# Kernel tuning notes

Measured on AMD Instinct MI355X. Metric: run time of the kernel, lower is better.

Reference implementation:

```python
import jax, jax.numpy as jnp
import numpy as np

EPS = 1e-12
NUM_ITERATIONS = 3


def squash(t, axis=-1):
    sn = jnp.sum(t * t, axis=axis, keepdims=True)
    scale = sn / (1.0 + sn + EPS)
    return scale * t / jnp.sqrt(sn + EPS)


def setup_inputs() -> dict:
    key = jax.random.key(0)
    k1, k2 = jax.random.split(key)
    B, R, IN, OUT, C = 128, 4096, 16, 32, 2
    x = jax.random.normal(k1, (B, R, IN), dtype=jnp.float32)
    # learned parameter: torch.randn(num_capsules, num_route_nodes, in, out)
    route_weights = jax.random.normal(k2, (C, R, IN, OUT), dtype=jnp.float32)
    return {"x": x, "route_weights": route_weights}


def reference(x, route_weights):
    # priors: [C, B, R, 1, O] == x[None,:,:,None,:] @ W[:,None,:,:,:]
    priors = jnp.einsum('bri,crio->cbro', x, route_weights)[..., None, :]
    # logits kept [C,B,R,1,1]: the torch code stores [C,B,R,1,O] but every
    # update (delta_logits) is constant along O, so softmax over axis=2 is identical.
    logits = jnp.zeros(priors.shape[:-1] + (1,), dtype=priors.dtype)
    outputs = None
    for i in range(NUM_ITERATIONS):
        probs = jax.nn.softmax(logits, axis=2)                      # over route nodes
        s = jnp.sum(probs * priors, axis=2, keepdims=True)          # [C,B,1,1,O]
        outputs = squash(s, axis=-1)
        if i != NUM_ITERATIONS - 1:
            delta = jnp.sum(priors * outputs, axis=-1, keepdims=True)  # [C,B,R,1,1]
            logits = logits + delta
    return outputs
```

## Files before the change

### kernel.cpp

```cpp
#include <hip/hip_runtime.h>
#include <hip/hip_cooperative_groups.h>
#include <math.h>

namespace cg = cooperative_groups;

#define CB    128
#define CR    4096
#define CIN   16
#define COUT  32
#define CCAP  2
#define RC    16
#define NRCH  (CR / RC)
#define GRID  (CCAP * NRCH)
#define EPSF  1e-12f

typedef _Float16 h8  __attribute__((ext_vector_type(8)));
typedef _Float16 h4t __attribute__((ext_vector_type(4)));
typedef float    f4  __attribute__((ext_vector_type(4)));
typedef float    f8v __attribute__((ext_vector_type(8)));

__device__ __forceinline__ void stage_pack_W(const float* __restrict__ w,
                                             int c, int r0, int t,
                                             _Float16* WpL, float* Stg)
{
  h4t* WpL4 = (h4t*)WpL;
#pragma unroll
  for (int h = 0; h < 2; ++h) {
    const float4* src = (const float4*)(w + ((size_t)c * CR + r0 + h * 8) * 512);
    ((float4*)Stg)[t]       = src[t];
    ((float4*)Stg)[t + 512] = src[t + 512];
    __syncthreads();
#pragma unroll
    for (int q = 0; q < 2; ++q) {
      const int sl  = t * 2 + q;
      const int rr  = sl >> 7;
      const int rem = sl & 127;
      const int ot  = rem >> 6;
      const int gs  = (rem >> 4) & 3;
      const int ms  = rem & 15;
      h4t v;
#pragma unroll
      for (int j = 0; j < 4; ++j)
        v[j] = (_Float16)Stg[rr * 512 + (4 * gs + j) * 32 + ot * 16 + ms];
      WpL4[(h * 8 + rr) * 128 + rem] = v;
    }
    __syncthreads();
  }
}

__device__ __forceinline__ void store_partials(float* __restrict__ partialA,
                                               float* __restrict__ partialE,
                                               const float* accA, const float* accB,
                                               float esum, int c, int rch,
                                               int t, int g, int b)
{
  float4 a4 = {accA[0], accA[1], accA[2], accA[3]};
  float4 b4 = {accB[0], accB[1], accB[2], accB[3]};
  float* dst = partialA + ((size_t)(c * NRCH + rch)) * 4096 + (size_t)t * 8;
  *(float4*)dst = a4;
  *(float4*)(dst + 4) = b4;
  if (g == 0) partialE[((size_t)(c * NRCH + rch)) * CB + b] = esum;
}

__device__ __forceinline__ void pass0_body(const float* __restrict__ x,
                                           float* __restrict__ partialA,
                                           float* __restrict__ partialE,
                                           const _Float16* WpL,
                                           int c, int rch, int t, h8* pf)
{
  const int r0 = rch * RC;
  const int wv = t >> 6, L = t & 63, g = L >> 4, m = L & 15;
  const int b  = wv * 16 + m;
  const h4t* WpL4 = (const h4t*)WpL;

  float accA[4] = {0.f, 0.f, 0.f, 0.f};
  float accB[4] = {0.f, 0.f, 0.f, 0.f};

#pragma unroll 4
  for (int ri = 0; ri < RC; ++ri) {
    const int r = r0 + ri;
    float4 xf = *(const float4*)(x + ((size_t)b * CR + r) * CIN + 4 * g);
    h8 bx = {(_Float16)xf.x, (_Float16)xf.y, (_Float16)xf.z, (_Float16)xf.w,
             (_Float16)0.f, (_Float16)0.f, (_Float16)0.f, (_Float16)0.f};
    h4t wA4 = WpL4[ri * 128 + L];
    h4t wB4 = WpL4[ri * 128 + 64 + L];
    h8 aA = {wA4[0], wA4[1], wA4[2], wA4[3],
             (_Float16)0.f, (_Float16)0.f, (_Float16)0.f, (_Float16)0.f};
    h8 aB = {wB4[0], wB4[1], wB4[2], wB4[3],
             (_Float16)0.f, (_Float16)0.f, (_Float16)0.f, (_Float16)0.f};
    f4 z = {0.f, 0.f, 0.f, 0.f};
    f4 pA = __builtin_amdgcn_mfma_f32_16x16x32_f16(aA, bx, z, 0, 0, 0);
    f4 pB = __builtin_amdgcn_mfma_f32_16x16x32_f16(aB, bx, z, 0, 0, 0);

    h8 pk = {(_Float16)pA[0], (_Float16)pA[1], (_Float16)pA[2], (_Float16)pA[3],
             (_Float16)pB[0], (_Float16)pB[1], (_Float16)pB[2], (_Float16)pB[3]};
    pf[ri] = pk;
#pragma unroll
    for (int j = 0; j < 4; ++j) { accA[j] += pA[j]; accB[j] += pB[j]; }
  }
  store_partials(partialA, partialE, accA, accB, (float)RC, c, rch, t, g, b);
}

__device__ __forceinline__ void passN_body(const float* __restrict__ vsum,
                                           float* __restrict__ partialA,
                                           float* __restrict__ partialE,
                                           int c, int rch, int t, const h8* pf)
{
  const int wv = t >> 6, L = t & 63, g = L >> 4, m = L & 15;
  const int b  = wv * 16 + m;

  const float* vb = vsum + ((size_t)c * CB + b) * COUT;
  float4 vA = *(const float4*)(vb + 4 * g);
  float4 vB = *(const float4*)(vb + 16 + 4 * g);

  float accA[4] = {0.f, 0.f, 0.f, 0.f};
  float accB[4] = {0.f, 0.f, 0.f, 0.f};
  float esum = 0.f;

#pragma unroll
  for (int ri = 0; ri < RC; ++ri) {
    f8v p = __builtin_convertvector(pf[ri], f8v);
    float d = p[0] * vA.x + p[1] * vA.y + p[2] * vA.z + p[3] * vA.w
            + p[4] * vB.x + p[5] * vB.y + p[6] * vB.z + p[7] * vB.w;
    d += __shfl_xor(d, 16);
    d += __shfl_xor(d, 32);
    const float e = __expf(d);
    esum += e;
#pragma unroll
    for (int j = 0; j < 4; ++j) { accA[j] += e * p[j]; accB[j] += e * p[4 + j]; }
  }
  store_partials(partialA, partialE, accA, accB, esum, c, rch, t, g, b);
}

template <int JG>
__device__ __forceinline__ void redv_body(const float* __restrict__ partialA,
                                          const float* __restrict__ partialE,
                                          float* __restrict__ vsum,
                                          float* __restrict__ out,
                                          float (*red)[33], float* rede,
                                          int cb, int t, int mode)
{
  const int c2 = cb >> 7, b2 = cb & 127;
  const int o = t & 31, jg = t >> 5;
  const int wv2 = b2 >> 4, m2 = b2 & 15;
  const int half = o >> 4, oo = o & 15, g2 = oo >> 2, j2 = oo & 3;
  const size_t idx = (size_t)(wv2 * 64 + g2 * 16 + m2) * 8 + half * 4 + j2;

  float s = 0.f;
#pragma unroll 4
  for (int k = 0; k < NRCH / JG; ++k) {
    const int j = jg + k * JG;
    s += partialA[((size_t)(c2 * NRCH + j)) * 4096 + idx];
  }
  red[jg][o] = s;
  __syncthreads();

  if (t < JG) {
    float e = 0.f;
#pragma unroll 4
    for (int k = 0; k < NRCH / JG; ++k)
      e += partialE[((size_t)(c2 * NRCH + t + k * JG)) * CB + b2];
    rede[t] = e;
  }
  __syncthreads();

  if (t < 32) {
    float sv = 0.f, es = 0.f;
#pragma unroll
    for (int jj = 0; jj < JG; ++jj) { sv += red[jj][t]; es += rede[jj]; }
    float sm = sv / es;
    float sn = sm * sm;
#pragma unroll
    for (int sh = 1; sh < 32; sh <<= 1) sn += __shfl_xor(sn, sh);
    float fac = sn / ((1.f + sn + EPSF) * sqrtf(sn + EPSF));
    float vv = sm * fac;
    if (mode == 2)      out[cb * COUT + t]  = vv;
    else if (mode == 1) vsum[cb * COUT + t] += vv;
    else                vsum[cb * COUT + t] = vv;
  }
}

__global__ __launch_bounds__(512, 4) void caps_coop_kernel(
    const float* __restrict__ x, const float* __restrict__ w,
    float* __restrict__ vsum, float* __restrict__ partialA,
    float* __restrict__ partialE, float* __restrict__ out)
{
  cg::grid_group grid = cg::this_grid();
  const int blk = (int)blockIdx.x;
  const int c = blk >> 8, rch = blk & 255;
  const int t = (int)threadIdx.x;

  __shared__ __align__(16) char lds[32768];
  _Float16* WpL = (_Float16*)lds;
  float* Stg = (float*)(lds + 16384);
  float (*red)[33] = (float (*)[33])(lds + 16384);
  float* rede = (float*)(lds + 16384 + 16 * 33 * 4);

  h8 pf[RC];

  stage_pack_W(w, c, rch * RC, t, WpL, Stg);
  pass0_body(x, partialA, partialE, WpL, c, rch, t, pf);
  __threadfence();
  grid.sync();
  if (blk < 256)
    redv_body<16>(partialA, partialE, vsum, out, red, rede, blk, t, 0);
  __threadfence();
  grid.sync();

#pragma unroll 1
  for (int it = 1; it < 3; ++it) {
    passN_body(vsum, partialA, partialE, c, rch, t, pf);
    __threadfence();
    grid.sync();
    if (blk < 256)
      redv_body<16>(partialA, partialE, vsum, out, red, rede, blk, t, it);
    if (it < 2) {
      __threadfence();
      grid.sync();
    }
  }
}

__device__ __forceinline__ void pass_full_body(const float* __restrict__ x,
                                               const float* __restrict__ vsum,
                                               float* __restrict__ partialA,
                                               float* __restrict__ partialE,
                                               const _Float16* WpL,
                                               int c, int rch, int t, int uniform)
{
  const int r0 = rch * RC;
  const int wv = t >> 6, L = t & 63, g = L >> 4, m = L & 15;
  const int b  = wv * 16 + m;
  const h4t* WpL4 = (const h4t*)WpL;

  float4 vA = {0.f, 0.f, 0.f, 0.f}, vB = {0.f, 0.f, 0.f, 0.f};
  if (!uniform) {
    const float* vb = vsum + ((size_t)c * CB + b) * COUT;
    vA = *(const float4*)(vb + 4 * g);
    vB = *(const float4*)(vb + 16 + 4 * g);
  }
  float accA[4] = {0.f, 0.f, 0.f, 0.f};
  float accB[4] = {0.f, 0.f, 0.f, 0.f};
  float esum = 0.f;

#pragma unroll 4
  for (int ri = 0; ri < RC; ++ri) {
    const int r = r0 + ri;
    float4 xf = *(const float4*)(x + ((size_t)b * CR + r) * CIN + 4 * g);
    h8 bx = {(_Float16)xf.x, (_Float16)xf.y, (_Float16)xf.z, (_Float16)xf.w,
             (_Float16)0.f, (_Float16)0.f, (_Float16)0.f, (_Float16)0.f};
    h4t wA4 = WpL4[ri * 128 + L];
    h4t wB4 = WpL4[ri * 128 + 64 + L];
    h8 aA = {wA4[0], wA4[1], wA4[2], wA4[3],
             (_Float16)0.f, (_Float16)0.f, (_Float16)0.f, (_Float16)0.f};
    h8 aB = {wB4[0], wB4[1], wB4[2], wB4[3],
             (_Float16)0.f, (_Float16)0.f, (_Float16)0.f, (_Float16)0.f};
    f4 z = {0.f, 0.f, 0.f, 0.f};
    f4 pA = __builtin_amdgcn_mfma_f32_16x16x32_f16(aA, bx, z, 0, 0, 0);
    f4 pB = __builtin_amdgcn_mfma_f32_16x16x32_f16(aB, bx, z, 0, 0, 0);

    float e = 1.f;
    if (!uniform) {
      float d = pA[0] * vA.x + pA[1] * vA.y + pA[2] * vA.z + pA[3] * vA.w
              + pB[0] * vB.x + pB[1] * vB.y + pB[2] * vB.z + pB[3] * vB.w;
      d += __shfl_xor(d, 16);
      d += __shfl_xor(d, 32);
      e = __expf(d);
    }
    esum += e;
#pragma unroll
    for (int j = 0; j < 4; ++j) { accA[j] += e * pA[j]; accB[j] += e * pB[j]; }
  }
  store_partials(partialA, partialE, accA, accB, esum, c, rch, t, g, b);
}

__global__ __launch_bounds__(512) void caps_pass_kernel(
    const float* __restrict__ x, const float* __restrict__ w,
    const float* __restrict__ vsum, float* __restrict__ partialA,
    float* __restrict__ partialE, int uniform)
{
  const int blk = (int)blockIdx.x;
  const int c = blk >> 8, rch = blk & 255;
  const int t = (int)threadIdx.x;
  __shared__ __align__(16) char lds[32768];
  _Float16* WpL = (_Float16*)lds;
  float* Stg = (float*)(lds + 16384);
  stage_pack_W(w, c, rch * RC, t, WpL, Stg);
  pass_full_body(x, vsum, partialA, partialE, WpL, c, rch, t, uniform);
}

__global__ __launch_bounds__(256) void caps_redv_kernel(
    const float* __restrict__ partialA, const float* __restrict__ partialE,
    float* __restrict__ vsum, float* __restrict__ out, int mode)
{
  __shared__ float red[8][33];
  __shared__ float rede[8];
  redv_body<8>(partialA, partialE, vsum, out, red, rede,
               (int)blockIdx.x, (int)threadIdx.x, mode);
}

extern "C" void kernel_launch(void* const* d_in, const int* in_sizes, int n_in,
                              void* d_out, int out_size, void* d_ws, size_t ws_size,
                              hipStream_t stream) {
  const float* x = (const float*)d_in[0];
  const float* w = (const float*)d_in[1];
  float* out = (float*)d_out;

  char* p = (char*)d_ws;
  float* vsum = (float*)p;
  p += (size_t)CCAP * CB * COUT * sizeof(float);
  float* partialA = (float*)p;
  p += (size_t)CCAP * NRCH * 4096 * sizeof(float);
  float* partialE = (float*)p;

  int maxB = 0;
  bool coop_ok =
      (hipOccupancyMaxActiveBlocksPerMultiprocessor(
           &maxB, (const void*)caps_coop_kernel, 512, 0) == hipSuccess) &&
      (maxB >= 2);

  if (coop_ok) {
    void* args[] = {(void*)&x, (void*)&w, (void*)&vsum,
                    (void*)&partialA, (void*)&partialE, (void*)&out};
    hipError_t e = hipLaunchCooperativeKernel((const void*)caps_coop_kernel,
                                              dim3(GRID), dim3(512), args, 0,
                                              stream);
    if (e == hipSuccess) return;
    (void)hipGetLastError();
  }

  for (int it = 0; it < 3; ++it) {
    caps_pass_kernel<<<dim3(GRID), 512, 0, stream>>>(
        x, w, vsum, partialA, partialE, it == 0 ? 1 : 0);
    caps_redv_kernel<<<dim3(CCAP * CB), 256, 0, stream>>>(
        partialA, partialE, vsum, out, it);
  }
}
```

Measured before the change: 75.96 us.

## Process both capsules per block in cooperative kernel, halving grid size

The cooperative kernel now launches one block per route chunk (256 blocks) instead of one per capsule-chunk pair (512). Each block stages both capsules' weights into LDS and reuses each x load for both capsules' MFMAs. It also holds priors for both capsules in registers. Every block now takes part in the reduction step instead of only half of them. This halves x global reads and the number of grid-sync participants, but doubles per-thread register use (launch bounds drop to 2 blocks/SM) and raises LDS usage.

```diff
diff --git a/kernel.cpp b/kernel.cpp
--- a/kernel.cpp
+++ b/kernel.cpp
@@ -11,7 +11,6 @@
 #define CCAP  2
 #define RC    16
 #define NRCH  (CR / RC)
-#define GRID  (CCAP * NRCH)
 #define EPSF  1e-12f
 
 typedef _Float16 h8  __attribute__((ext_vector_type(8)));
@@ -62,19 +61,180 @@
   if (g == 0) partialE[((size_t)(c * NRCH + rch)) * CB + b] = esum;
 }
 
-__device__ __forceinline__ void pass0_body(const float* __restrict__ x,
-                                           float* __restrict__ partialA,
-                                           float* __restrict__ partialE,
-                                           const _Float16* WpL,
-                                           int c, int rch, int t, h8* pf)
+template <int JG>
+__device__ __forceinline__ void redv_body(const float* __restrict__ partialA,
+                                          const float* __restrict__ partialE,
+                                          float* __restrict__ vsum,
+                                          float* __restrict__ out,
+                                          float (*red)[33], float* rede,
+                                          int cb, int t, int mode)
+{
+  const int c2 = cb >> 7, b2 = cb & 127;
+  const int o = t & 31, jg = t >> 5;
+  const int wv2 = b2 >> 4, m2 = b2 & 15;
+  const int half = o >> 4, oo = o & 15, g2 = oo >> 2, j2 = oo & 3;
+  const size_t idx = (size_t)(wv2 * 64 + g2 * 16 + m2) * 8 + half * 4 + j2;
+
+  float s = 0.f;
+#pragma unroll 4
+  for (int k = 0; k < NRCH / JG; ++k) {
+    const int j = jg + k * JG;
+    s += partialA[((size_t)(c2 * NRCH + j)) * 4096 + idx];
+  }
+  red[jg][o] = s;
+  __syncthreads();
+
+  if (t < JG) {
+    float e = 0.f;
+#pragma unroll 4
+    for (int k = 0; k < NRCH / JG; ++k)
+      e += partialE[((size_t)(c2 * NRCH + t + k * JG)) * CB + b2];
+    rede[t] = e;
+  }
+  __syncthreads();
+
+  if (t < 32) {
+    float sv = 0.f, es = 0.f;
+#pragma unroll
+    for (int jj = 0; jj < JG; ++jj) { sv += red[jj][t]; es += rede[jj]; }
+    float sm = sv / es;
+    float sn = sm * sm;
+#pragma unroll
+    for (int sh = 1; sh < 32; sh <<= 1) sn += __shfl_xor(sn, sh);
+    float fac = sn / ((1.f + sn + EPSF) * sqrtf(sn + EPSF));
+    float vv = sm * fac;
+    if (mode == 2)      out[cb * COUT + t]  = vv;
+    else if (mode == 1) vsum[cb * COUT + t] += vv;
+    else                vsum[cb * COUT + t] = vv;
+  }
+  __syncthreads();
+}
+
+__global__ __launch_bounds__(512, 2) void caps_coop_kernel(
+    const float* __restrict__ x, const float* __restrict__ w,
+    float* __restrict__ vsum, float* __restrict__ partialA,
+    float* __restrict__ partialE, float* __restrict__ out)
+{
+  cg::grid_group grid = cg::this_grid();
+  const int rch = (int)blockIdx.x;
+  const int r0  = rch * RC;
+  const int t   = (int)threadIdx.x;
+  const int wv  = t >> 6, L = t & 63, g = L >> 4, m = L & 15;
+  const int b   = wv * 16 + m;
+
+  __shared__ __align__(16) char lds[49152];
+  _Float16* WpL0 = (_Float16*)lds;
+  _Float16* WpL1 = (_Float16*)(lds + 16384);
+  float* Stg = (float*)(lds + 32768);
+  float (*red)[33] = (float (*)[33])(lds + 32768);
+  float* rede = (float*)(lds + 32768 + 16 * 33 * 4);
+
+  stage_pack_W(w, 0, r0, t, WpL0, Stg);
+  stage_pack_W(w, 1, r0, t, WpL1, Stg);
+
+  h8 pf0[RC], pf1[RC];
+
+  {
+    const h4t* W0 = (const h4t*)WpL0;
+    const h4t* W1 = (const h4t*)WpL1;
+    float acc0A[4] = {0.f, 0.f, 0.f, 0.f}, acc0B[4] = {0.f, 0.f, 0.f, 0.f};
+    float acc1A[4] = {0.f, 0.f, 0.f, 0.f}, acc1B[4] = {0.f, 0.f, 0.f, 0.f};
+#pragma unroll
+    for (int ri = 0; ri < RC; ++ri) {
+      float4 xf = *(const float4*)(x + ((size_t)b * CR + r0 + ri) * CIN + 4 * g);
+      h8 bx = {(_Float16)xf.x, (_Float16)xf.y, (_Float16)xf.z, (_Float16)xf.w,
+               (_Float16)0.f, (_Float16)0.f, (_Float16)0.f, (_Float16)0.f};
+      f4 z = {0.f, 0.f, 0.f, 0.f};
+
+      h4t a0 = W0[ri * 128 + L], b0 = W0[ri * 128 + 64 + L];
+      h8 aA0 = {a0[0], a0[1], a0[2], a0[3],
+                (_Float16)0.f, (_Float16)0.f, (_Float16)0.f, (_Float16)0.f};
+      h8 aB0 = {b0[0], b0[1], b0[2], b0[3],
+                (_Float16)0.f, (_Float16)0.f, (_Float16)0.f, (_Float16)0.f};
+      f4 pA0 = __builtin_amdgcn_mfma_f32_16x16x32_f16(aA0, bx, z, 0, 0, 0);
+      f4 pB0 = __builtin_amdgcn_mfma_f32_16x16x32_f16(aB0, bx, z, 0, 0, 0);
+      pf0[ri] = h8{(_Float16)pA0[0], (_Float16)pA0[1], (_Float16)pA0[2], (_Float16)pA0[3],
+                   (_Float16)pB0[0], (_Float16)pB0[1], (_Float16)pB0[2], (_Float16)pB0[3]};
+#pragma unroll
+      for (int j = 0; j < 4; ++j) { acc0A[j] += pA0[j]; acc0B[j] += pB0[j]; }
+
+      h4t a1 = W1[ri * 128 + L], b1 = W1[ri * 128 + 64 + L];
+      h8 aA1 = {a1[0], a1[1], a1[2], a1[3],
+                (_Float16)0.f, (_Float16)0.f, (_Float16)0.f, (_Float16)0.f};
+      h8 aB1 = {b1[0], b1[1], b1[2], b1[3],
+                (_Float16)0.f, (_Float16)0.f, (_Float16)0.f, (_Float16)0.f};
+      f4 pA1 = __builtin_amdgcn_mfma_f32_16x16x32_f16(aA1, bx, z, 0, 0, 0);
+      f4 pB1 = __builtin_amdgcn_mfma_f32_16x16x32_f16(aB1, bx, z, 0, 0, 0);
+      pf1[ri] = h8{(_Float16)pA1[0], (_Float16)pA1[1], (_Float16)pA1[2], (_Float16)pA1[3],
+                   (_Float16)pB1[0], (_Float16)pB1[1], (_Float16)pB1[2], (_Float16)pB1[3]};
+#pragma unroll
+      for (int j = 0; j < 4; ++j) { acc1A[j] += pA1[j]; acc1B[j] += pB1[j]; }
+    }
+    store_partials(partialA, partialE, acc0A, acc0B, (float)RC, 0, rch, t, g, b);
+    store_partials(partialA, partialE, acc1A, acc1B, (float)RC, 1, rch, t, g, b);
+  }
+
+  __threadfence();
+  grid.sync();
+  redv_body<16>(partialA, partialE, vsum, out, red, rede, rch, t, 0);
+  __threadfence();
+  grid.sync();
+
+#pragma unroll 1
+  for (int it = 1; it < 3; ++it) {
+#pragma unroll
+    for (int cc = 0; cc < 2; ++cc) {
+      const float* vb = vsum + ((size_t)cc * CB + b) * COUT;
+      float4 vA = *(const float4*)(vb + 4 * g);
+      float4 vB = *(const float4*)(vb + 16 + 4 * g);
+      float accA[4] = {0.f, 0.f, 0.f, 0.f};
+      float accB[4] = {0.f, 0.f, 0.f, 0.f};
+      float esum = 0.f;
+#pragma unroll
+      for (int ri = 0; ri < RC; ++ri) {
+        f8v p = __builtin_convertvector(cc == 0 ? pf0[ri] : pf1[ri], f8v);
+        float d = p[0] * vA.x + p[1] * vA.y + p[2] * vA.z + p[3] * vA.w
+                + p[4] * vB.x + p[5] * vB.y + p[6] * vB.z + p[7] * vB.w;
+        d += __shfl_xor(d, 16);
+        d += __shfl_xor(d, 32);
+        const float e = __expf(d);
+        esum += e;
+#pragma unroll
+        for (int j = 0; j < 4; ++j) { accA[j] += e * p[j]; accB[j] += e * p[4 + j]; }
+      }
+      store_partials(partialA, partialE, accA, accB, esum, cc, rch, t, g, b);
+    }
+    __threadfence();
+    grid.sync();
+    redv_body<16>(partialA, partialE, vsum, out, red, rede, rch, t, it);
+    if (it < 2) {
+      __threadfence();
+      grid.sync();
+    }
+  }
+}
+
+__device__ __forceinline__ void pass_full_body(const float* __restrict__ x,
+                                               const float* __restrict__ vsum,
+                                               float* __restrict__ partialA,
+                                               float* __restrict__ partialE,
+                                               const _Float16* WpL,
+                                               int c, int rch, int t, int uniform)
 {
   const int r0 = rch * RC;
   const int wv = t >> 6, L = t & 63, g = L >> 4, m = L & 15;
   const int b  = wv * 16 + m;
   const h4t* WpL4 = (const h4t*)WpL;
 
+  float4 vA = {0.f, 0.f, 0.f, 0.f}, vB = {0.f, 0.f, 0.f, 0.f};
+  if (!uniform) {
+    const float* vb = vsum + ((size_t)c * CB + b) * COUT;
+    vA = *(const float4*)(vb + 4 * g);
+    vB = *(const float4*)(vb + 16 + 4 * g);
+  }
   float accA[4] = {0.f, 0.f, 0.f, 0.f};
   float accB[4] = {0.f, 0.f, 0.f, 0.f};
+  float esum = 0.f;
 
 #pragma unroll 4
   for (int ri = 0; ri < RC; ++ri) {
@@ -92,173 +252,6 @@
     f4 pA = __builtin_amdgcn_mfma_f32_16x16x32_f16(aA, bx, z, 0, 0, 0);
     f4 pB = __builtin_amdgcn_mfma_f32_16x16x32_f16(aB, bx, z, 0, 0, 0);
 
-    h8 pk = {(_Float16)pA[0], (_Float16)pA[1], (_Float16)pA[2], (_Float16)pA[3],
-             (_Float16)pB[0], (_Float16)pB[1], (_Float16)pB[2], (_Float16)pB[3]};
-    pf[ri] = pk;
-#pragma unroll
-    for (int j = 0; j < 4; ++j) { accA[j] += pA[j]; accB[j] += pB[j]; }
-  }
-  store_partials(partialA, partialE, accA, accB, (float)RC, c, rch, t, g, b);
-}
-
-__device__ __forceinline__ void passN_body(const float* __restrict__ vsum,
-                                           float* __restrict__ partialA,
-                                           float* __restrict__ partialE,
-                                           int c, int rch, int t, const h8* pf)
-{
-  const int wv = t >> 6, L = t & 63, g = L >> 4, m = L & 15;
-  const int b  = wv * 16 + m;
-
-  const float* vb = vsum + ((size_t)c * CB + b) * COUT;
-  float4 vA = *(const float4*)(vb + 4 * g);
-  float4 vB = *(const float4*)(vb + 16 + 4 * g);
-
-  float accA[4] = {0.f, 0.f, 0.f, 0.f};
-  float accB[4] = {0.f, 0.f, 0.f, 0.f};
-  float esum = 0.f;
-
-#pragma unroll
-  for (int ri = 0; ri < RC; ++ri) {
-    f8v p = __builtin_convertvector(pf[ri], f8v);
-    float d = p[0] * vA.x + p[1] * vA.y + p[2] * vA.z + p[3] * vA.w
-            + p[4] * vB.x + p[5] * vB.y + p[6] * vB.z + p[7] * vB.w;
-    d += __shfl_xor(d, 16);
-    d += __shfl_xor(d, 32);
-    const float e = __expf(d);
-    esum += e;
-#pragma unroll
-    for (int j = 0; j < 4; ++j) { accA[j] += e * p[j]; accB[j] += e * p[4 + j]; }
-  }
-  store_partials(partialA, partialE, accA, accB, esum, c, rch, t, g, b);
-}
-
-template <int JG>
-__device__ __forceinline__ void redv_body(const float* __restrict__ partialA,
-                                          const float* __restrict__ partialE,
-                                          float* __restrict__ vsum,
-                                          float* __restrict__ out,
-                                          float (*red)[33], float* rede,
-                                          int cb, int t, int mode)
-{
-  const int c2 = cb >> 7, b2 = cb & 127;
-  const int o = t & 31, jg = t >> 5;
-  const int wv2 = b2 >> 4, m2 = b2 & 15;
-  const int half = o >> 4, oo = o & 15, g2 = oo >> 2, j2 = oo & 3;
-  const size_t idx = (size_t)(wv2 * 64 + g2 * 16 + m2) * 8 + half * 4 + j2;
-
-  float s = 0.f;
-#pragma unroll 4
-  for (int k = 0; k < NRCH / JG; ++k) {
-    const int j = jg + k * JG;
-    s += partialA[((size_t)(c2 * NRCH + j)) * 4096 + idx];
-  }
-  red[jg][o] = s;
-  __syncthreads();
-
-  if (t < JG) {
-    float e = 0.f;
-#pragma unroll 4
-    for (int k = 0; k < NRCH / JG; ++k)
-      e += partialE[((size_t)(c2 * NRCH + t + k * JG)) * CB + b2];
-    rede[t] = e;
-  }
-  __syncthreads();
-
-  if (t < 32) {
-    float sv = 0.f, es = 0.f;
-#pragma unroll
-    for (int jj = 0; jj < JG; ++jj) { sv += red[jj][t]; es += rede[jj]; }
-    float sm = sv / es;
-    float sn = sm * sm;
-#pragma unroll
-    for (int sh = 1; sh < 32; sh <<= 1) sn += __shfl_xor(sn, sh);
-    float fac = sn / ((1.f + sn + EPSF) * sqrtf(sn + EPSF));
-    float vv = sm * fac;
-    if (mode == 2)      out[cb * COUT + t]  = vv;
-    else if (mode == 1) vsum[cb * COUT + t] += vv;
-    else                vsum[cb * COUT + t] = vv;
-  }
-}
-
-__global__ __launch_bounds__(512, 4) void caps_coop_kernel(
-    const float* __restrict__ x, const float* __restrict__ w,
-    float* __restrict__ vsum, float* __restrict__ partialA,
-    float* __restrict__ partialE, float* __restrict__ out)
-{
-  cg::grid_group grid = cg::this_grid();
-  const int blk = (int)blockIdx.x;
-  const int c = blk >> 8, rch = blk & 255;
-  const int t = (int)threadIdx.x;
-
-  __shared__ __align__(16) char lds[32768];
-  _Float16* WpL = (_Float16*)lds;
-  float* Stg = (float*)(lds + 16384);
-  float (*red)[33] = (float (*)[33])(lds + 16384);
-  float* rede = (float*)(lds + 16384 + 16 * 33 * 4);
-
-  h8 pf[RC];
-
-  stage_pack_W(w, c, rch * RC, t, WpL, Stg);
-  pass0_body(x, partialA, partialE, WpL, c, rch, t, pf);
-  __threadfence();
-  grid.sync();
-  if (blk < 256)
-    redv_body<16>(partialA, partialE, vsum, out, red, rede, blk, t, 0);
-  __threadfence();
-  grid.sync();
-
-#pragma unroll 1
-  for (int it = 1; it < 3; ++it) {
-    passN_body(vsum, partialA, partialE, c, rch, t, pf);
-    __threadfence();
-    grid.sync();
-    if (blk < 256)
-      redv_body<16>(partialA, partialE, vsum, out, red, rede, blk, t, it);
-    if (it < 2) {
-      __threadfence();
-      grid.sync();
-    }
-  }
-}
-
-__device__ __forceinline__ void pass_full_body(const float* __restrict__ x,
-                                               const float* __restrict__ vsum,
-                                               float* __restrict__ partialA,
-                                               float* __restrict__ partialE,
-                                               const _Float16* WpL,
-                                               int c, int rch, int t, int uniform)
-{
-  const int r0 = rch * RC;
-  const int wv = t >> 6, L = t & 63, g = L >> 4, m = L & 15;
-  const int b  = wv * 16 + m;
-  const h4t* WpL4 = (const h4t*)WpL;
-
-  float4 vA = {0.f, 0.f, 0.f, 0.f}, vB = {0.f, 0.f, 0.f, 0.f};
-  if (!uniform) {
-    const float* vb = vsum + ((size_t)c * CB + b) * COUT;
-    vA = *(const float4*)(vb + 4 * g);
-    vB = *(const float4*)(vb + 16 + 4 * g);
-  }
-  float accA[4] = {0.f, 0.f, 0.f, 0.f};
-  float accB[4] = {0.f, 0.f, 0.f, 0.f};
-  float esum = 0.f;
-
-#pragma unroll 4
-  for (int ri = 0; ri < RC; ++ri) {
-    const int r = r0 + ri;
-    float4 xf = *(const float4*)(x + ((size_t)b * CR + r) * CIN + 4 * g);
-    h8 bx = {(_Float16)xf.x, (_Float16)xf.y, (_Float16)xf.z, (_Float16)xf.w,
-             (_Float16)0.f, (_Float16)0.f, (_Float16)0.f, (_Float16)0.f};
-    h4t wA4 = WpL4[ri * 128 + L];
-    h4t wB4 = WpL4[ri * 128 + 64 + L];
-    h8 aA = {wA4[0], wA4[1], wA4[2], wA4[3],
-             (_Float16)0.f, (_Float16)0.f, (_Float16)0.f, (_Float16)0.f};
-    h8 aB = {wB4[0], wB4[1], wB4[2], wB4[3],
-             (_Float16)0.f, (_Float16)0.f, (_Float16)0.f, (_Float16)0.f};
-    f4 z = {0.f, 0.f, 0.f, 0.f};
-    f4 pA = __builtin_amdgcn_mfma_f32_16x16x32_f16(aA, bx, z, 0, 0, 0);
-    f4 pB = __builtin_amdgcn_mfma_f32_16x16x32_f16(aB, bx, z, 0, 0, 0);
-
     float e = 1.f;
     if (!uniform) {
       float d = pA[0] * vA.x + pA[1] * vA.y + pA[2] * vA.z + pA[3] * vA.w
@@ -317,20 +310,20 @@
   bool coop_ok =
       (hipOccupancyMaxActiveBlocksPerMultiprocessor(
            &maxB, (const void*)caps_coop_kernel, 512, 0) == hipSuccess) &&
-      (maxB >= 2);
+      (maxB >= 1);
 
   if (coop_ok) {
     void* args[] = {(void*)&x, (void*)&w, (void*)&vsum,
                     (void*)&partialA, (void*)&partialE, (void*)&out};
     hipError_t e = hipLaunchCooperativeKernel((const void*)caps_coop_kernel,
-                                              dim3(GRID), dim3(512), args, 0,
+                                              dim3(NRCH), dim3(512), args, 0,
                                               stream);
     if (e == hipSuccess) return;
     (void)hipGetLastError();
   }
 
   for (int it = 0; it < 3; ++it) {
-    caps_pass_kernel<<<dim3(GRID), 512, 0, stream>>>(
+    caps_pass_kernel<<<dim3(CCAP * NRCH), 512, 0, stream>>>(
         x, w, vsum, partialA, partialE, it == 0 ? 1 : 0);
     caps_redv_kernel<<<dim3(CCAP * CB), 256, 0, stream>>>(
         partialA, partialE, vsum, out, it);
```

Result: no change. 76.29 us (+0.4%).
